# Kernel tuning notes

Hardware: AMD Instinct MI355X
Metric: run time of the kernel (lower is better)

## Reference

```python
import jax, jax.numpy as jnp
import numpy as np

N = 262144          # ray samples
L = 16              # grid levels
T = 2 ** 19         # hash table entries per level
F = 2               # features per entry
NMIN, NMAX = 16, 2048
SB = 1.0            # scene_bound
DW, CW = 64, 64     # density / color MLP widths

_PRIMES = jnp.array([1, 2654435761, 805459861], dtype=jnp.uint32)
_OFFS = jnp.asarray(np.stack(np.meshgrid([0, 1], [0, 1], [0, 1], indexing='ij'), -1).reshape(8, 3), dtype=jnp.uint32)  # 8 cube corners


def _scalings():
    g = np.exp((np.log(NMAX) - np.log(NMIN)) / (L - 1))
    return jnp.asarray(np.floor(NMIN * g ** np.arange(L)), dtype=jnp.float32)  # (L,)


def hash_encode(pos01, table):
    # pos01: (N,3) in [0,1]; table: (L*T, F)
    scaled = pos01[:, None, :] * _scalings()[None, :, None]        # (N,L,3)
    floor = jnp.floor(scaled)
    frac = scaled - floor                                          # (N,L,3)
    corners = floor.astype(jnp.uint32)[:, :, None, :] + _OFFS[None, None]  # (N,L,8,3)
    h = corners * _PRIMES                                          # uint32 wraparound hashing
    idx = (h[..., 0] ^ h[..., 1] ^ h[..., 2]) % jnp.uint32(T)      # (N,L,8)
    idx = idx.astype(jnp.int32) + (jnp.arange(L, dtype=jnp.int32) * T)[None, :, None]
    feats = table[idx]                                             # (N,L,8,F) gather
    sel = _OFFS.astype(bool)[None, None]                           # (1,1,8,3)
    w = jnp.prod(jnp.where(sel, frac[:, :, None, :], 1.0 - frac[:, :, None, :]), axis=-1)  # (N,L,8)
    out = jnp.einsum('nlcf,nlc->nlf', feats, w)                    # trilinear interp
    return out.reshape(out.shape[0], L * F)                        # (N, 32)


def sh_encode(d):
    # 4th-order real spherical harmonics, 16 components (instant-ngp convention)
    x, y, z = d[..., 0], d[..., 1], d[..., 2]
    xx, yy, zz = x * x, y * y, z * z
    xy, yz, xz = x * y, y * z, x * z
    return jnp.stack([
        jnp.full_like(x, 0.28209479177387814),
        -0.48860251190291987 * y,
        0.48860251190291987 * z,
        -0.48860251190291987 * x,
        1.0925484305920792 * xy,
        -1.0925484305920792 * yz,
        0.94617469575755997 * zz - 0.31539156525252005,
        -1.0925484305920792 * xz,
        0.54627421529603959 * (xx - yy),
        0.59004358992664352 * y * (-3.0 * xx + yy),
        2.8906114426405538 * xy * z,
        0.45704579946446572 * y * (1.0 - 5.0 * zz),
        0.3731763325901154 * z * (5.0 * zz - 3.0),
        0.45704579946446572 * x * (1.0 - 5.0 * zz),
        1.445305721320277 * z * (xx - yy),
        0.59004358992664352 * x * (xx - 3.0 * yy),
    ], axis=-1)  # (N,16)


def setup_inputs() -> dict:
    key = jax.random.key(0)
    ks = jax.random.split(key, 10)
    position = jax.random.uniform(ks[0], (N, 3), jnp.float32, -SB, SB)
    d = jax.random.normal(ks[1], (N, 3), jnp.float32)
    direction = d / jnp.linalg.norm(d, axis=-1, keepdims=True)
    hash_table = jax.random.uniform(ks[2], (L * T, F), jnp.float32, -1e-4, 1e-4)
    def dense(k, fin, fout, std):
        return (jax.random.normal(k, (fin, fout), jnp.float32) * std,
                jnp.zeros((fout,), jnp.float32))
    w1, b1 = dense(ks[3], L * F, DW, 0.01)      # normal() init in source
    w2, b2 = dense(ks[4], DW, 16, 0.01)
    w3, b3 = dense(ks[5], 16 + 16, CW, 0.01)
    w4, b4 = dense(ks[6], CW, CW, 0.01)
    w5, b5 = dense(ks[7], CW, 3, 0.1)           # default lecun-ish scale
    return dict(position=position, direction=direction, hash_table=hash_table,
                w1=w1, b1=b1, w2=w2, b2=b2, w3=w3, b3=b3, w4=w4, b4=b4, w5=w5, b5=b5)


def reference(position, direction, hash_table, w1, b1, w2, b2, w3, b3, w4, b4, w5, b5):
    p = (position + SB) / (2.0 * SB)                 # -> [0,1]
    enc = hash_encode(p, hash_table)                 # (N,32)
    h = jax.nn.relu(enc @ w1 + b1)                   # density MLP
    h = h @ w2 + b2                                  # (N,16)
    density = jnp.exp(h[:, 0:1])                     # exponential_density_activation
    sh = sh_encode(direction)                        # (N,16)
    c = jnp.concatenate([h, sh], axis=-1)            # (N,32)
    c = jax.nn.relu(c @ w3 + b3)
    c = jax.nn.relu(c @ w4 + b4)
    c = c @ w5 + b5
    color = jax.nn.sigmoid(c)                        # high_dynamic_range=False
    return jnp.concatenate([density, color], axis=-1)  # (N,4) drgbs
```

## Files before the change

kernel.cpp:

```cpp
#include <hip/hip_runtime.h>
#include <cmath>

namespace {
constexpr int kN = 262144;
constexpr int kL = 16;
constexpr int kT = 1 << 19;
constexpr unsigned kTMask = kT - 1;
constexpr int kB = 32768;

typedef __attribute__((ext_vector_type(8))) short short8;
typedef __attribute__((ext_vector_type(4))) float f32x4;
typedef __attribute__((ext_vector_type(4))) unsigned short ushort4v;

struct Scales { float s[kL]; };

__device__ __forceinline__ unsigned short f2bf(float f) {
    unsigned u = __builtin_bit_cast(unsigned, f);
    return (unsigned short)((u + 0x7FFFu + ((u >> 16) & 1u)) >> 16);
}

__device__ __forceinline__ unsigned morton5(unsigned x) {
    x &= 31u;
    x = (x | (x << 8)) & 0x100Fu;
    x = (x | (x << 4)) & 0x10C3u;
    x = (x | (x << 2)) & 0x1249u;
    return x;
}

__global__ __launch_bounds__(256) void prep_w(
    const float* __restrict__ w1, const float* __restrict__ w2,
    const float* __restrict__ w3, const float* __restrict__ w4,
    const float* __restrict__ w5, unsigned short* __restrict__ out)
{
    const int i = blockIdx.x * 256 + threadIdx.x;
    const int f = i >> 9;
    const int l = (i >> 3) & 63;
    const int e = i & 7;
    const int cl = l & 15;
    const int kg = l >> 4;
    float v = 0.0f;
    if (f < 4) {
        v = w1[(kg * 8 + e) * 64 + f * 16 + cl];
    } else if (f < 6) {
        const int q = f - 4;
        v = w2[(q * 32 + kg * 8 + e) * 16 + cl];
    } else if (f < 10) {
        v = w3[(kg * 8 + e) * 64 + (f - 6) * 16 + cl];
    } else if (f < 18) {
        const int g = f - 10, q = g >> 2, nt = g & 3;
        v = w4[(q * 32 + kg * 8 + e) * 64 + nt * 16 + cl];
    } else {
        const int q = f - 18;
        v = (cl < 3) ? w5[(q * 32 + kg * 8 + e) * 3 + cl] : 0.0f;
    }
    out[i] = f2bf(v);
}

__global__ __launch_bounds__(256) void bucket_hist(
    const float* __restrict__ pos,
    unsigned short* __restrict__ key,
    unsigned* __restrict__ hist)
{
    const int n = blockIdx.x * 256 + threadIdx.x;
    const float px = (pos[n * 3 + 0] + 1.0f) * 0.5f;
    const float py = (pos[n * 3 + 1] + 1.0f) * 0.5f;
    const float pz = (pos[n * 3 + 2] + 1.0f) * 0.5f;
    const unsigned cx = (unsigned)min(31, (int)(px * 32.0f));
    const unsigned cy = (unsigned)min(31, (int)(py * 32.0f));
    const unsigned cz = (unsigned)min(31, (int)(pz * 32.0f));
    const unsigned k = morton5(cx) | (morton5(cy) << 1) | (morton5(cz) << 2);
    key[n] = (unsigned short)k;
    atomicAdd(&hist[k], 1u);
}

__global__ __launch_bounds__(1024) void bucket_scan(
    const unsigned* __restrict__ hist,
    unsigned* __restrict__ cursor)
{
    __shared__ unsigned s[1024];
    const int t = threadIdx.x;
    unsigned sum = 0;
    #pragma unroll 4
    for (int i = 0; i < 32; ++i) sum += hist[t * 32 + i];
    s[t] = sum;
    __syncthreads();
    for (int off = 1; off < 1024; off <<= 1) {
        unsigned x = (t >= off) ? s[t - off] : 0u;
        __syncthreads();
        s[t] += x;
        __syncthreads();
    }
    unsigned base = (t > 0) ? s[t - 1] : 0u;
    #pragma unroll 4
    for (int i = 0; i < 32; ++i) {
        const unsigned h = hist[t * 32 + i];
        cursor[t * 32 + i] = base;
        base += h;
    }
}

__global__ __launch_bounds__(256) void bucket_scatter(
    const float* __restrict__ pos,
    const unsigned short* __restrict__ key,
    unsigned* __restrict__ cursor,
    float4* __restrict__ spos4,
    unsigned* __restrict__ s2o)
{
    const int n = blockIdx.x * 256 + threadIdx.x;
    const unsigned k = key[n];
    const unsigned i = atomicAdd(&cursor[k], 1u);
    spos4[i] = make_float4(pos[n * 3 + 0], pos[n * 3 + 1], pos[n * 3 + 2],
                           __uint_as_float((unsigned)n));
    s2o[i] = (unsigned)n;
}

__global__ __launch_bounds__(256) void ngp_encode(
    const float4* __restrict__ spos4,
    const float2* __restrict__ table,
    unsigned* __restrict__ enc,
    Scales sc)
{
    const int bid = blockIdx.x;
    const int l = bid >> 10;
    const int n = ((bid & 1023) << 8) | threadIdx.x;

    const float s = sc.s[l];
    const float2* __restrict__ tl = table + (size_t)l * kT;

    const float4 p4 = spos4[n];
    const float px = (p4.x + 1.0f) * 0.5f;
    const float py = (p4.y + 1.0f) * 0.5f;
    const float pz = (p4.z + 1.0f) * 0.5f;
    const float sx = px * s, sy = py * s, sz = pz * s;
    const float fx = floorf(sx), fy = floorf(sy), fz = floorf(sz);
    const float rx = sx - fx, ry = sy - fy, rz = sz - fz;
    const unsigned cx = (unsigned)fx, cy = (unsigned)fy, cz = (unsigned)fz;

    const unsigned hy0 = cy * 2654435761u, hy1 = (cy + 1u) * 2654435761u;
    const unsigned hz0 = cz * 805459861u,  hz1 = (cz + 1u) * 805459861u;

    float4 pr[4];
    float2 ex[4];
    unsigned idx0v[4], hyzv[4];

    #pragma unroll
    for (int j = 0; j < 4; ++j) {
        const unsigned hyz = ((j >> 1) ? hy1 : hy0) ^ ((j & 1) ? hz1 : hz0);
        hyzv[j] = hyz;
        const unsigned idx0 = (cx ^ hyz) & kTMask;
        idx0v[j] = idx0;
        pr[j] = *reinterpret_cast<const float4*>(tl + (idx0 & ~1u));
    }

    if (cx & 1u) {
        const unsigned cx1 = cx + 1u;
        #pragma unroll
        for (int j = 0; j < 4; ++j)
            ex[j] = tl[(cx1 ^ hyzv[j]) & kTMask];
    }

    const bool odd = (cx & 1u) != 0u;
    const float wx0 = 1.0f - rx, wx1 = rx;
    float f0 = 0.f, f1 = 0.f;
    #pragma unroll
    for (int j = 0; j < 4; ++j) {
        const float wyz = ((j >> 1) ? ry : 1.0f - ry) *
                          ((j & 1) ? rz : 1.0f - rz);
        const bool hi = (idx0v[j] & 1u) != 0u;
        const float c0x = hi ? pr[j].z : pr[j].x;
        const float c0y = hi ? pr[j].w : pr[j].y;
        const float c1x = odd ? ex[j].x : (hi ? pr[j].x : pr[j].z);
        const float c1y = odd ? ex[j].y : (hi ? pr[j].y : pr[j].w);
        f0 = fmaf(c0x, wx0 * wyz, f0);
        f1 = fmaf(c0y, wx0 * wyz, f1);
        f0 = fmaf(c1x, wx1 * wyz, f0);
        f1 = fmaf(c1y, wx1 * wyz, f1);
    }
    enc[(size_t)l * kN + n] = (unsigned)f2bf(f0) | ((unsigned)f2bf(f1) << 16);
}

__global__ __launch_bounds__(256) void ngp_mlp_mfma(
    const unsigned* __restrict__ enc,
    const unsigned short* __restrict__ wbf,
    const float* __restrict__ dir,
    const unsigned* __restrict__ s2o,
    const float* __restrict__ b1, const float* __restrict__ b2,
    const float* __restrict__ b3, const float* __restrict__ b4,
    const float* __restrict__ b5,
    float* __restrict__ out)
{
    __shared__ unsigned short sA[4][4096];
    __shared__ unsigned short sB[4][2048];

    const int tid = threadIdx.x;
    const int wid = tid >> 6;
    const int l   = tid & 63;
    const int cl  = l & 15;
    const int kg  = l >> 4;
    unsigned short* __restrict__ A_ = sA[wid];
    unsigned short* __restrict__ B_ = sB[wid];
    const int gbase = blockIdx.x * 256 + wid * 64;

    {
        const unsigned n = s2o[gbase + l];
        const float x = dir[n * 3 + 0], y = dir[n * 3 + 1], z = dir[n * 3 + 2];
        const float xx = x * x, yy = y * y, zz = z * z;
        const float xy = x * y, yz = y * z, xz = x * z;
        float sh[16];
        sh[0] = 0.28209479177387814f;
        sh[1] = -0.48860251190291987f * y;
        sh[2] = 0.48860251190291987f * z;
        sh[3] = -0.48860251190291987f * x;
        sh[4] = 1.0925484305920792f * xy;
        sh[5] = -1.0925484305920792f * yz;
        sh[6] = 0.94617469575755997f * zz - 0.31539156525252005f;
        sh[7] = -1.0925484305920792f * xz;
        sh[8] = 0.54627421529603959f * (xx - yy);
        sh[9] = 0.59004358992664352f * y * (-3.0f * xx + yy);
        sh[10] = 2.8906114426405538f * xy * z;
        sh[11] = 0.45704579946446572f * y * (1.0f - 5.0f * zz);
        sh[12] = 0.3731763325901154f * z * (5.0f * zz - 3.0f);
        sh[13] = 0.45704579946446572f * x * (1.0f - 5.0f * zz);
        sh[14] = 1.445305721320277f * z * (xx - yy);
        sh[15] = 0.59004358992664352f * x * (xx - 3.0f * yy);
        #pragma unroll
        for (int j = 0; j < 16; ++j)
            B_[(l >> 4) * 512 + (16 + j) * 16 + (l & 15)] = f2bf(sh[j]);
    }

    short8 A1[4];
    #pragma unroll
    for (int m = 0; m < 4; ++m) {
        #pragma unroll
        for (int j = 0; j < 4; ++j) {
            const unsigned v = enc[(size_t)(kg * 4 + j) * kN + (gbase + m * 16 + cl)];
            A1[m][2 * j]     = (short)(v & 0xFFFFu);
            A1[m][2 * j + 1] = (short)(v >> 16);
        }
    }
    {
        short8 B1[4];
        #pragma unroll
        for (int nt = 0; nt < 4; ++nt)
            B1[nt] = *reinterpret_cast<const short8*>(&wbf[(size_t)(nt) * 512 + l * 8]);

        f32x4 acc[4][4];
        #pragma unroll
        for (int nt = 0; nt < 4; ++nt) {
            const float bv = b1[nt * 16 + cl];
            #pragma unroll
            for (int m = 0; m < 4; ++m) {
                acc[m][nt][0] = bv; acc[m][nt][1] = bv; acc[m][nt][2] = bv; acc[m][nt][3] = bv;
            }
        }
        #pragma unroll
        for (int m = 0; m < 4; ++m)
            #pragma unroll
            for (int nt = 0; nt < 4; ++nt)
                acc[m][nt] = __builtin_amdgcn_mfma_f32_16x16x32_bf16(A1[m], B1[nt], acc[m][nt], 0, 0, 0);

        #pragma unroll
        for (int m = 0; m < 4; ++m) {
            #pragma unroll
            for (int nt = 0; nt < 4; ++nt) {
                ushort4v pk;
                #pragma unroll
                for (int r = 0; r < 4; ++r) pk[r] = f2bf(fmaxf(acc[m][nt][r], 0.0f));
                *reinterpret_cast<ushort4v*>(&A_[m * 1024 + (nt * 16 + cl) * 16 + kg * 4]) = pk;
            }
        }
    }

    {
        short8 A2[4][2];
        #pragma unroll
        for (int m = 0; m < 4; ++m)
            #pragma unroll
            for (int q = 0; q < 2; ++q)
                #pragma unroll
                for (int e = 0; e < 8; ++e)
                    A2[m][q][e] = (short)A_[m * 1024 + (q * 32 + kg * 8 + e) * 16 + cl];

        short8 B2[2];
        #pragma unroll
        for (int q = 0; q < 2; ++q)
            B2[q] = *reinterpret_cast<const short8*>(&wbf[(size_t)(4 + q) * 512 + l * 8]);

        f32x4 acc[4];
        const float bv = b2[cl];
        #pragma unroll
        for (int m = 0; m < 4; ++m) { acc[m][0] = bv; acc[m][1] = bv; acc[m][2] = bv; acc[m][3] = bv; }
        #pragma unroll
        for (int m = 0; m < 4; ++m)
            #pragma unroll
            for (int q = 0; q < 2; ++q)
                acc[m] = __builtin_amdgcn_mfma_f32_16x16x32_bf16(A2[m][q], B2[q], acc[m], 0, 0, 0);

        #pragma unroll
        for (int m = 0; m < 4; ++m) {
            if (cl == 0) {
                #pragma unroll
                for (int r = 0; r < 4; ++r)
                    out[(size_t)s2o[gbase + m * 16 + kg * 4 + r] * 4 + 0] = expf(acc[m][r]);
            }
            ushort4v pk;
            #pragma unroll
            for (int r = 0; r < 4; ++r) pk[r] = f2bf(acc[m][r]);
            *reinterpret_cast<ushort4v*>(&B_[m * 512 + cl * 16 + kg * 4]) = pk;
        }
    }

    {
        short8 A3[4];
        #pragma unroll
        for (int m = 0; m < 4; ++m)
            #pragma unroll
            for (int e = 0; e < 8; ++e)
                A3[m][e] = (short)B_[m * 512 + (kg * 8 + e) * 16 + cl];

        short8 B3[4];
        #pragma unroll
        for (int nt = 0; nt < 4; ++nt)
            B3[nt] = *reinterpret_cast<const short8*>(&wbf[(size_t)(6 + nt) * 512 + l * 8]);

        f32x4 acc[4][4];
        #pragma unroll
        for (int nt = 0; nt < 4; ++nt) {
            const float bv = b3[nt * 16 + cl];
            #pragma unroll
            for (int m = 0; m < 4; ++m) {
                acc[m][nt][0] = bv; acc[m][nt][1] = bv; acc[m][nt][2] = bv; acc[m][nt][3] = bv;
            }
        }
        #pragma unroll
        for (int m = 0; m < 4; ++m)
            #pragma unroll
            for (int nt = 0; nt < 4; ++nt)
                acc[m][nt] = __builtin_amdgcn_mfma_f32_16x16x32_bf16(A3[m], B3[nt], acc[m][nt], 0, 0, 0);

        #pragma unroll
        for (int m = 0; m < 4; ++m) {
            #pragma unroll
            for (int nt = 0; nt < 4; ++nt) {
                ushort4v pk;
                #pragma unroll
                for (int r = 0; r < 4; ++r) pk[r] = f2bf(fmaxf(acc[m][nt][r], 0.0f));
                *reinterpret_cast<ushort4v*>(&A_[m * 1024 + (nt * 16 + cl) * 16 + kg * 4]) = pk;
            }
        }
    }

    {
        short8 A4[4][2];
        #pragma unroll
        for (int m = 0; m < 4; ++m)
            #pragma unroll
            for (int q = 0; q < 2; ++q)
                #pragma unroll
                for (int e = 0; e < 8; ++e)
                    A4[m][q][e] = (short)A_[m * 1024 + (q * 32 + kg * 8 + e) * 16 + cl];

        short8 B4[2][4];
        #pragma unroll
        for (int q = 0; q < 2; ++q)
            #pragma unroll
            for (int nt = 0; nt < 4; ++nt)
                B4[q][nt] = *reinterpret_cast<const short8*>(&wbf[(size_t)(10 + q * 4 + nt) * 512 + l * 8]);

        f32x4 acc[4][4];
        #pragma unroll
        for (int nt = 0; nt < 4; ++nt) {
            const float bv = b4[nt * 16 + cl];
            #pragma unroll
            for (int m = 0; m < 4; ++m) {
                acc[m][nt][0] = bv; acc[m][nt][1] = bv; acc[m][nt][2] = bv; acc[m][nt][3] = bv;
            }
        }
        #pragma unroll
        for (int m = 0; m < 4; ++m)
            #pragma unroll
            for (int nt = 0; nt < 4; ++nt)
                #pragma unroll
                for (int q = 0; q < 2; ++q)
                    acc[m][nt] = __builtin_amdgcn_mfma_f32_16x16x32_bf16(A4[m][q], B4[q][nt], acc[m][nt], 0, 0, 0);

        #pragma unroll
        for (int m = 0; m < 4; ++m) {
            #pragma unroll
            for (int nt = 0; nt < 4; ++nt) {
                ushort4v pk;
                #pragma unroll
                for (int r = 0; r < 4; ++r) pk[r] = f2bf(fmaxf(acc[m][nt][r], 0.0f));
                *reinterpret_cast<ushort4v*>(&A_[m * 1024 + (nt * 16 + cl) * 16 + kg * 4]) = pk;
            }
        }
    }

    {
        short8 A5[4][2];
        #pragma unroll
        for (int m = 0; m < 4; ++m)
            #pragma unroll
            for (int q = 0; q < 2; ++q)
                #pragma unroll
                for (int e = 0; e < 8; ++e)
                    A5[m][q][e] = (short)A_[m * 1024 + (q * 32 + kg * 8 + e) * 16 + cl];

        short8 B5[2];
        #pragma unroll
        for (int q = 0; q < 2; ++q)
            B5[q] = *reinterpret_cast<const short8*>(&wbf[(size_t)(18 + q) * 512 + l * 8]);

        f32x4 acc[4];
        const float bv = (cl < 3) ? b5[cl] : 0.0f;
        #pragma unroll
        for (int m = 0; m < 4; ++m) { acc[m][0] = bv; acc[m][1] = bv; acc[m][2] = bv; acc[m][3] = bv; }
        #pragma unroll
        for (int m = 0; m < 4; ++m)
            #pragma unroll
            for (int q = 0; q < 2; ++q)
                acc[m] = __builtin_amdgcn_mfma_f32_16x16x32_bf16(A5[m][q], B5[q], acc[m], 0, 0, 0);

        if (cl < 3) {
            #pragma unroll
            for (int m = 0; m < 4; ++m)
                #pragma unroll
                for (int r = 0; r < 4; ++r)
                    out[(size_t)s2o[gbase + m * 16 + kg * 4 + r] * 4 + 1 + cl] =
                        1.0f / (1.0f + expf(-acc[m][r]));
        }
    }
}

}

extern "C" void kernel_launch(void* const* d_in, const int* in_sizes, int n_in,
                              void* d_out, int out_size, void* d_ws, size_t ws_size,
                              hipStream_t stream) {
    (void)in_sizes; (void)n_in; (void)out_size; (void)ws_size;

    Scales sc;
    const double g = exp((log(2048.0) - log(16.0)) / 15.0);
    for (int l = 0; l < kL; ++l) sc.s[l] = (float)floor(16.0 * pow(g, (double)l));

    const float*  pos   = (const float*)d_in[0];
    const float*  dir   = (const float*)d_in[1];
    const float2* table = (const float2*)d_in[2];
    const float *w1 = (const float*)d_in[3],  *b1 = (const float*)d_in[4];
    const float *w2 = (const float*)d_in[5],  *b2 = (const float*)d_in[6];
    const float *w3 = (const float*)d_in[7],  *b3 = (const float*)d_in[8];
    const float *w4 = (const float*)d_in[9],  *b4 = (const float*)d_in[10];
    const float *w5 = (const float*)d_in[11], *b5 = (const float*)d_in[12];
    float* out = (float*)d_out;

    char* ws = (char*)d_ws;
    unsigned short* wbf    = (unsigned short*)(ws);
    unsigned*       hist   = (unsigned*)(ws + 65536);
    unsigned*       cursor = (unsigned*)(ws + 196608);
    unsigned short* key    = (unsigned short*)(ws + 327680);
    unsigned*       s2o    = (unsigned*)(ws + 851968);
    float4*         spos4  = (float4*)(ws + 1966080);
    unsigned*       enc    = (unsigned*)(ws + 6291456);

    hipMemsetAsync(hist, 0, kB * sizeof(unsigned), stream);
    prep_w<<<40, 256, 0, stream>>>(w1, w2, w3, w4, w5, wbf);
    bucket_hist<<<kN / 256, 256, 0, stream>>>(pos, key, hist);
    bucket_scan<<<1, 1024, 0, stream>>>(hist, cursor);
    bucket_scatter<<<kN / 256, 256, 0, stream>>>(pos, key, cursor, spos4, s2o);
    ngp_encode<<<kL * 1024, 256, 0, stream>>>(spos4, table, enc, sc);
    ngp_mlp_mfma<<<kN / 256, 256, 0, stream>>>(enc, wbf, dir, s2o,
        b1, b2, b3, b4, b5, out);
}
```

Baseline: 164.9 us.

## Replace global-atomic bucket sort with LDS-histogram counting sort over 4096 cells

Rebuilds the spatial Morton bucketing as a two-level counting sort. Each of 64 blocks builds a per-block histogram in shared memory, a column pass computes per-block offsets, a single-block scan produces the bucket bases, and a scatter pass ranks points with shared-memory atomics. The grid is also coarsened from 32^3 to 16^3 cells. This removes contended global atomics and the memset, but runs the hist and scatter passes on only 64 blocks, and the coarser cells may reduce gather locality in the encode stage.

Result: faster. 146.2 us (-11.4%).

```diff
diff --git a/kernel.cpp b/kernel.cpp
--- a/kernel.cpp
+++ b/kernel.cpp
@@ -6,7 +6,8 @@
 constexpr int kL = 16;
 constexpr int kT = 1 << 19;
 constexpr unsigned kTMask = kT - 1;
-constexpr int kB = 32768;
+constexpr int kB = 4096;
+constexpr int kSB = 64;
 
 typedef __attribute__((ext_vector_type(8))) short short8;
 typedef __attribute__((ext_vector_type(4))) float f32x4;
@@ -25,6 +26,16 @@
     x = (x | (x << 4)) & 0x10C3u;
     x = (x | (x << 2)) & 0x1249u;
     return x;
+}
+
+__device__ __forceinline__ unsigned morton_key16(float x, float y, float z) {
+    const float px = (x + 1.0f) * 0.5f;
+    const float py = (y + 1.0f) * 0.5f;
+    const float pz = (z + 1.0f) * 0.5f;
+    const unsigned cx = (unsigned)min(15, (int)(px * 16.0f));
+    const unsigned cy = (unsigned)min(15, (int)(py * 16.0f));
+    const unsigned cz = (unsigned)min(15, (int)(pz * 16.0f));
+    return morton5(cx) | (morton5(cy) << 1) | (morton5(cz) << 2);
 }
 
 __global__ __launch_bounds__(256) void prep_w(
@@ -56,32 +67,51 @@
     out[i] = f2bf(v);
 }
 
-__global__ __launch_bounds__(256) void bucket_hist(
+__global__ __launch_bounds__(1024) void hist_lds(
     const float* __restrict__ pos,
-    unsigned short* __restrict__ key,
-    unsigned* __restrict__ hist)
-{
-    const int n = blockIdx.x * 256 + threadIdx.x;
-    const float px = (pos[n * 3 + 0] + 1.0f) * 0.5f;
-    const float py = (pos[n * 3 + 1] + 1.0f) * 0.5f;
-    const float pz = (pos[n * 3 + 2] + 1.0f) * 0.5f;
-    const unsigned cx = (unsigned)min(31, (int)(px * 32.0f));
-    const unsigned cy = (unsigned)min(31, (int)(py * 32.0f));
-    const unsigned cz = (unsigned)min(31, (int)(pz * 32.0f));
-    const unsigned k = morton5(cx) | (morton5(cy) << 1) | (morton5(cz) << 2);
-    key[n] = (unsigned short)k;
-    atomicAdd(&hist[k], 1u);
-}
-
-__global__ __launch_bounds__(1024) void bucket_scan(
-    const unsigned* __restrict__ hist,
+    unsigned* __restrict__ h2)
+{
+    __shared__ unsigned lh[kB];
+    const int t = threadIdx.x;
+    #pragma unroll
+    for (int i = 0; i < 4; ++i) lh[t + i * 1024] = 0u;
+    __syncthreads();
+    const int base = blockIdx.x * 4096;
+    #pragma unroll
+    for (int i = 0; i < 4; ++i) {
+        const int n = base + t + i * 1024;
+        atomicAdd(&lh[morton_key16(pos[n * 3 + 0], pos[n * 3 + 1], pos[n * 3 + 2])], 1u);
+    }
+    __syncthreads();
+    #pragma unroll
+    for (int i = 0; i < 4; ++i)
+        h2[(size_t)blockIdx.x * kB + t + i * 1024] = lh[t + i * 1024];
+}
+
+__global__ __launch_bounds__(256) void boff_k(
+    const unsigned* __restrict__ h2,
+    unsigned* __restrict__ boff,
+    unsigned* __restrict__ total)
+{
+    const int k = blockIdx.x * 256 + threadIdx.x;
+    unsigned acc = 0;
+    #pragma unroll 8
+    for (int b = 0; b < kSB; ++b) {
+        const unsigned v = h2[(size_t)b * kB + k];
+        boff[(size_t)b * kB + k] = acc;
+        acc += v;
+    }
+    total[k] = acc;
+}
+
+__global__ __launch_bounds__(1024) void scan4096(
+    const unsigned* __restrict__ total,
     unsigned* __restrict__ cursor)
 {
     __shared__ unsigned s[1024];
     const int t = threadIdx.x;
-    unsigned sum = 0;
-    #pragma unroll 4
-    for (int i = 0; i < 32; ++i) sum += hist[t * 32 + i];
+    const uint4 v = reinterpret_cast<const uint4*>(total)[t];
+    const unsigned sum = v.x + v.y + v.z + v.w;
     s[t] = sum;
     __syncthreads();
     for (int off = 1; off < 1024; off <<= 1) {
@@ -90,28 +120,39 @@
         s[t] += x;
         __syncthreads();
     }
-    unsigned base = (t > 0) ? s[t - 1] : 0u;
-    #pragma unroll 4
-    for (int i = 0; i < 32; ++i) {
-        const unsigned h = hist[t * 32 + i];
-        cursor[t * 32 + i] = base;
-        base += h;
-    }
-}
-
-__global__ __launch_bounds__(256) void bucket_scatter(
+    const unsigned base = (t > 0) ? s[t - 1] : 0u;
+    uint4 c;
+    c.x = base;
+    c.y = base + v.x;
+    c.z = base + v.x + v.y;
+    c.w = base + v.x + v.y + v.z;
+    reinterpret_cast<uint4*>(cursor)[t] = c;
+}
+
+__global__ __launch_bounds__(1024) void scatter_lds(
     const float* __restrict__ pos,
-    const unsigned short* __restrict__ key,
-    unsigned* __restrict__ cursor,
+    const unsigned* __restrict__ boff,
+    const unsigned* __restrict__ cursor,
     float4* __restrict__ spos4,
     unsigned* __restrict__ s2o)
 {
-    const int n = blockIdx.x * 256 + threadIdx.x;
-    const unsigned k = key[n];
-    const unsigned i = atomicAdd(&cursor[k], 1u);
-    spos4[i] = make_float4(pos[n * 3 + 0], pos[n * 3 + 1], pos[n * 3 + 2],
-                           __uint_as_float((unsigned)n));
-    s2o[i] = (unsigned)n;
+    __shared__ unsigned lh[kB];
+    const int t = threadIdx.x;
+    #pragma unroll
+    for (int i = 0; i < 4; ++i) lh[t + i * 1024] = 0u;
+    __syncthreads();
+    const int base = blockIdx.x * 4096;
+    const unsigned* __restrict__ bo = boff + (size_t)blockIdx.x * kB;
+    #pragma unroll
+    for (int i = 0; i < 4; ++i) {
+        const int n = base + t + i * 1024;
+        const float x = pos[n * 3 + 0], y = pos[n * 3 + 1], z = pos[n * 3 + 2];
+        const unsigned k = morton_key16(x, y, z);
+        const unsigned r = atomicAdd(&lh[k], 1u);
+        const unsigned slot = cursor[k] + bo[k] + r;
+        spos4[slot] = make_float4(x, y, z, 0.0f);
+        s2o[slot] = (unsigned)n;
+    }
 }
 
 __global__ __launch_bounds__(256) void ngp_encode(
@@ -455,18 +496,19 @@
 
     char* ws = (char*)d_ws;
     unsigned short* wbf    = (unsigned short*)(ws);
-    unsigned*       hist   = (unsigned*)(ws + 65536);
-    unsigned*       cursor = (unsigned*)(ws + 196608);
-    unsigned short* key    = (unsigned short*)(ws + 327680);
-    unsigned*       s2o    = (unsigned*)(ws + 851968);
-    float4*         spos4  = (float4*)(ws + 1966080);
-    unsigned*       enc    = (unsigned*)(ws + 6291456);
-
-    hipMemsetAsync(hist, 0, kB * sizeof(unsigned), stream);
+    unsigned*       h2     = (unsigned*)(ws + 65536);
+    unsigned*       boff   = (unsigned*)(ws + 1114112);
+    unsigned*       total  = (unsigned*)(ws + 2162688);
+    unsigned*       cursor = (unsigned*)(ws + 2179072);
+    unsigned*       s2o    = (unsigned*)(ws + 2195456);
+    float4*         spos4  = (float4*)(ws + 3244032);
+    unsigned*       enc    = (unsigned*)(ws + 7438336);
+
     prep_w<<<40, 256, 0, stream>>>(w1, w2, w3, w4, w5, wbf);
-    bucket_hist<<<kN / 256, 256, 0, stream>>>(pos, key, hist);
-    bucket_scan<<<1, 1024, 0, stream>>>(hist, cursor);
-    bucket_scatter<<<kN / 256, 256, 0, stream>>>(pos, key, cursor, spos4, s2o);
+    hist_lds<<<kSB, 1024, 0, stream>>>(pos, h2);
+    boff_k<<<kB / 256, 256, 0, stream>>>(h2, boff, total);
+    scan4096<<<1, 1024, 0, stream>>>(total, cursor);
+    scatter_lds<<<kSB, 1024, 0, stream>>>(pos, boff, cursor, spos4, s2o);
     ngp_encode<<<kL * 1024, 256, 0, stream>>>(spos4, table, enc, sc);
     ngp_mlp_mfma<<<kN / 256, 256, 0, stream>>>(enc, wbf, dir, s2o,
         b1, b2, b3, b4, b5, out);
```
